# Kernel optimization log

Hardware: AMD Instinct MI355X
Metric: run time of the kernel (lower is better)

## Reference

```python
import jax, jax.numpy as jnp
import numpy as np

B, S, H = 64, 2048, 1024

def setup_inputs() -> dict:
    key = jax.random.key(0)
    k1, k2 = jax.random.split(key)
    enc_output = jax.random.normal(k1, (B, S, H), dtype=jnp.float32)
    h_n = jax.random.normal(k2, (B, H), dtype=jnp.float32)
    return {"enc_output": enc_output, "h_n": h_n}

def reference(enc_output, h_n):
    # dec_output: [B, 1, H]
    dec_output = h_n[:, None, :]
    # scores: [B, 1, S] = dec_output @ enc_output^T
    scores = jnp.einsum('bqh,bsh->bqs', dec_output, enc_output)
    attn = jax.nn.softmax(scores, axis=2)  # softmax over S
    # context: [B, 1, H] = attn @ enc_output
    context = jnp.einsum('bqs,bsh->bqh', attn, enc_output)
    # concat decoder state and attention context: [B, 1, 2H]
    return jnp.concatenate((dec_output, context), axis=2)
```

## Files before the change

kernel.cpp:

```cpp
#include <hip/hip_runtime.h>
#include <math.h>


#define BB 64
#define SS 2048
#define HH 1024
#define NCHUNK 16
#define SCHUNK (SS / NCHUNK)
#define NWAVE 4

typedef float fvec4 __attribute__((ext_vector_type(4)));

#define WS_ML_OFF ((size_t)BB * NCHUNK * HH)

__global__ __launch_bounds__(256) void attn_partial_kernel(
    const float* __restrict__ enc, const float* __restrict__ hn,
    float* __restrict__ ws)
{
    const int blk   = blockIdx.x;
    const int b     = blk / NCHUNK;
    const int chunk = blk % NCHUNK;
    const int tid   = threadIdx.x;
    const int wave  = tid >> 6;
    const int lane  = tid & 63;

    const fvec4* hn4 = (const fvec4*)(hn + (size_t)b * HH);
    fvec4 h4[4];
#pragma unroll
    for (int j = 0; j < 4; ++j) h4[j] = hn4[j * 64 + lane];

    const fvec4* enc4 = (const fvec4*)(enc + (size_t)b * SS * HH);

    float m = -INFINITY;
    float l = 0.0f;
    fvec4 acc[4];
#pragma unroll
    for (int j = 0; j < 4; ++j) acc[j] = (fvec4)(0.f, 0.f, 0.f, 0.f);

    const int s0    = chunk * SCHUNK;
    const int start = (blk * 53) & (SCHUNK - 1);

    for (int k = 0; k < SCHUNK / NWAVE; ++k) {
        const int r = (start + wave + NWAVE * k) & (SCHUNK - 1);
        const fvec4* row = enc4 + (size_t)(s0 + r) * (HH / 4);
        fvec4 e[4];
#pragma unroll
        for (int j = 0; j < 4; ++j)
            e[j] = __builtin_nontemporal_load(&row[j * 64 + lane]);

        float d = 0.0f;
#pragma unroll
        for (int j = 0; j < 4; ++j) {
            d += e[j].x * h4[j].x + e[j].y * h4[j].y
               + e[j].z * h4[j].z + e[j].w * h4[j].w;
        }
#pragma unroll
        for (int off = 32; off > 0; off >>= 1)
            d += __shfl_xor(d, off, 64);

        const float m_new = fmaxf(m, d);
        const float scale = __expf(m - m_new);
        const float p     = __expf(d - m_new);
        l = l * scale + p;
#pragma unroll
        for (int j = 0; j < 4; ++j) {
            acc[j].x = acc[j].x * scale + p * e[j].x;
            acc[j].y = acc[j].y * scale + p * e[j].y;
            acc[j].z = acc[j].z * scale + p * e[j].z;
            acc[j].w = acc[j].w * scale + p * e[j].w;
        }
        m = m_new;
    }

    __shared__ float s_m[NWAVE];
    __shared__ float s_l[NWAVE];
    __shared__ float s_acc[NWAVE][HH];

#pragma unroll
    for (int j = 0; j < 4; ++j)
        ((fvec4*)s_acc[wave])[j * 64 + lane] = acc[j];
    if (lane == 0) { s_m[wave] = m; s_l[wave] = l; }
    __syncthreads();

    float M = fmaxf(fmaxf(s_m[0], s_m[1]), fmaxf(s_m[2], s_m[3]));
    float sc[NWAVE];
    float L = 0.0f;
#pragma unroll
    for (int w = 0; w < NWAVE; ++w) {
        sc[w] = __expf(s_m[w] - M);
        L += s_l[w] * sc[w];
    }

    fvec4 ctx = (fvec4)(0.f, 0.f, 0.f, 0.f);
#pragma unroll
    for (int w = 0; w < NWAVE; ++w) {
        fvec4 a = ((const fvec4*)s_acc[w])[tid];
        ctx.x += sc[w] * a.x;  ctx.y += sc[w] * a.y;
        ctx.z += sc[w] * a.z;  ctx.w += sc[w] * a.w;
    }
    ((fvec4*)(ws + (size_t)blk * HH))[tid] = ctx;
    if (tid == 0) {
        ws[WS_ML_OFF + (size_t)blk * 2 + 0] = M;
        ws[WS_ML_OFF + (size_t)blk * 2 + 1] = L;
    }
}

__global__ __launch_bounds__(256) void attn_final_kernel(
    const float* __restrict__ hn, const float* __restrict__ ws,
    float* __restrict__ out)
{
    const int b   = blockIdx.x;
    const int tid = threadIdx.x;
    const float* ml = ws + WS_ML_OFF + (size_t)b * NCHUNK * 2;

    float M = -INFINITY;
#pragma unroll
    for (int c = 0; c < NCHUNK; ++c) M = fmaxf(M, ml[c * 2]);

    float sc[NCHUNK];
    float T = 0.0f;
#pragma unroll
    for (int c = 0; c < NCHUNK; ++c) {
        sc[c] = __expf(ml[c * 2] - M);
        T += sc[c] * ml[c * 2 + 1];
    }
    const float invT = 1.0f / T;

    fvec4 ctx = (fvec4)(0.f, 0.f, 0.f, 0.f);
#pragma unroll
    for (int c = 0; c < NCHUNK; ++c) {
        fvec4 a = ((const fvec4*)(ws + (size_t)(b * NCHUNK + c) * HH))[tid];
        ctx.x += sc[c] * a.x;  ctx.y += sc[c] * a.y;
        ctx.z += sc[c] * a.z;  ctx.w += sc[c] * a.w;
    }
    ctx.x *= invT; ctx.y *= invT; ctx.z *= invT; ctx.w *= invT;

    const fvec4 dec = ((const fvec4*)(hn + (size_t)b * HH))[tid];
    fvec4* o = (fvec4*)(out + (size_t)b * 2 * HH);
    o[tid]            = dec;
    o[tid + (HH / 4)] = ctx;
}

extern "C" void kernel_launch(void* const* d_in, const int* in_sizes, int n_in,
                              void* d_out, int out_size, void* d_ws, size_t ws_size,
                              hipStream_t stream) {
    const float* enc = (const float*)d_in[0];
    const float* hn  = (const float*)d_in[1];
    float* out = (float*)d_out;
    float* ws  = (float*)d_ws;

    attn_partial_kernel<<<dim3(BB * NCHUNK), dim3(256), 0, stream>>>(enc, hn, ws);
    attn_final_kernel<<<dim3(BB), dim3(256), 0, stream>>>(hn, ws, out);
}
```

Measured before the change: 642.2 us.

## Double-buffer row pairs and skip rescale when running max unchanged

Measured after the change: 644.4 us. About the same (+0.4%).

```diff
diff --git a/kernel.cpp b/kernel.cpp
--- a/kernel.cpp
+++ b/kernel.cpp
@@ -8,10 +8,63 @@
 #define NCHUNK 16
 #define SCHUNK (SS / NCHUNK)
 #define NWAVE 4
+#define NPAIR (SCHUNK / (2 * NWAVE))
 
 typedef float fvec4 __attribute__((ext_vector_type(4)));
 
 #define WS_ML_OFF ((size_t)BB * NCHUNK * HH)
+
+#define LOADP(kk, E0, E1) do {                                              \
+    const int pp_ = wave + NWAVE * (kk);                                    \
+    const int r0_ = (start + 2 * pp_)     & (SCHUNK - 1);                   \
+    const int r1_ = (start + 2 * pp_ + 1) & (SCHUNK - 1);                   \
+    const fvec4* R0_ = enc4 + (size_t)(s0 + r0_) * (HH / 4);                \
+    const fvec4* R1_ = enc4 + (size_t)(s0 + r1_) * (HH / 4);                \
+    _Pragma("unroll")                                                       \
+    for (int j = 0; j < 4; ++j) {                                           \
+        E0[j] = __builtin_nontemporal_load(&R0_[j * 64 + lane]);            \
+        E1[j] = __builtin_nontemporal_load(&R1_[j * 64 + lane]);            \
+    }                                                                       \
+} while (0)
+
+#define DOT4(E, j) (E[j].x * h4[j].x + E[j].y * h4[j].y                     \
+                  + E[j].z * h4[j].z + E[j].w * h4[j].w)
+
+#define CONSUME(E0, E1) do {                                                \
+    float d0_ = DOT4(E0, 0) + DOT4(E0, 1) + DOT4(E0, 2) + DOT4(E0, 3);     \
+    float d1_ = DOT4(E1, 0) + DOT4(E1, 1) + DOT4(E1, 2) + DOT4(E1, 3);     \
+    _Pragma("unroll")                                                       \
+    for (int off_ = 32; off_ > 0; off_ >>= 1) {                             \
+        d0_ += __shfl_xor(d0_, off_, 64);                                   \
+        d1_ += __shfl_xor(d1_, off_, 64);                                   \
+    }                                                                       \
+    const float pm_ = fmaxf(d0_, d1_);                                      \
+    if (pm_ <= m) {             \
+        const float p0_ = __expf(d0_ - m);                                  \
+        const float p1_ = __expf(d1_ - m);                                  \
+        l += p0_ + p1_;                                                     \
+        _Pragma("unroll")                                                   \
+        for (int j = 0; j < 4; ++j) {                                       \
+            acc[j].x = fmaf(p0_, E0[j].x, fmaf(p1_, E1[j].x, acc[j].x));    \
+            acc[j].y = fmaf(p0_, E0[j].y, fmaf(p1_, E1[j].y, acc[j].y));    \
+            acc[j].z = fmaf(p0_, E0[j].z, fmaf(p1_, E1[j].z, acc[j].z));    \
+            acc[j].w = fmaf(p0_, E0[j].w, fmaf(p1_, E1[j].w, acc[j].w));    \
+        }                                                                   \
+    } else {                    \
+        const float sc_ = __expf(m - pm_);     \
+        const float p0_ = __expf(d0_ - pm_);                                \
+        const float p1_ = __expf(d1_ - pm_);                                \
+        l = l * sc_ + p0_ + p1_;                                            \
+        m = pm_;                                                            \
+        _Pragma("unroll")                                                   \
+        for (int j = 0; j < 4; ++j) {                                       \
+            acc[j].x = fmaf(acc[j].x, sc_, fmaf(p0_, E0[j].x, p1_ * E1[j].x)); \
+            acc[j].y = fmaf(acc[j].y, sc_, fmaf(p0_, E0[j].y, p1_ * E1[j].y)); \
+            acc[j].z = fmaf(acc[j].z, sc_, fmaf(p0_, E0[j].z, p1_ * E1[j].z)); \
+            acc[j].w = fmaf(acc[j].w, sc_, fmaf(p0_, E0[j].w, p1_ * E1[j].w)); \
+        }                                                                   \
+    }                                                                       \
+} while (0)
 
 __global__ __launch_bounds__(256) void attn_partial_kernel(
     const float* __restrict__ enc, const float* __restrict__ hn,
@@ -40,37 +93,19 @@
     const int s0    = chunk * SCHUNK;
     const int start = (blk * 53) & (SCHUNK - 1);
 
-    for (int k = 0; k < SCHUNK / NWAVE; ++k) {
-        const int r = (start + wave + NWAVE * k) & (SCHUNK - 1);
-        const fvec4* row = enc4 + (size_t)(s0 + r) * (HH / 4);
-        fvec4 e[4];
+    fvec4 eA0[4], eA1[4], eB0[4], eB1[4];
+
+    LOADP(0, eA0, eA1);
 #pragma unroll
-        for (int j = 0; j < 4; ++j)
-            e[j] = __builtin_nontemporal_load(&row[j * 64 + lane]);
-
-        float d = 0.0f;
-#pragma unroll
-        for (int j = 0; j < 4; ++j) {
-            d += e[j].x * h4[j].x + e[j].y * h4[j].y
-               + e[j].z * h4[j].z + e[j].w * h4[j].w;
-        }
-#pragma unroll
-        for (int off = 32; off > 0; off >>= 1)
-            d += __shfl_xor(d, off, 64);
-
-        const float m_new = fmaxf(m, d);
-        const float scale = __expf(m - m_new);
-        const float p     = __expf(d - m_new);
-        l = l * scale + p;
-#pragma unroll
-        for (int j = 0; j < 4; ++j) {
-            acc[j].x = acc[j].x * scale + p * e[j].x;
-            acc[j].y = acc[j].y * scale + p * e[j].y;
-            acc[j].z = acc[j].z * scale + p * e[j].z;
-            acc[j].w = acc[j].w * scale + p * e[j].w;
-        }
-        m = m_new;
+    for (int k = 0; k < NPAIR / 2 - 1; ++k) {
+        LOADP(2 * k + 1, eB0, eB1);
+        CONSUME(eA0, eA1);
+        LOADP(2 * k + 2, eA0, eA1);
+        CONSUME(eB0, eB1);
     }
+    LOADP(NPAIR - 1, eB0, eB1);
+    CONSUME(eA0, eA1);
+    CONSUME(eB0, eB1);
 
     __shared__ float s_m[NWAVE];
     __shared__ float s_l[NWAVE];
```

## Double chunk count, give each wave a contiguous row run, branch online softmax

Applied to the files above, without the earlier changes.

Measured after the change: 659.2 us. +2.7%, slower.

```diff
diff --git a/kernel.cpp b/kernel.cpp
--- a/kernel.cpp
+++ b/kernel.cpp
@@ -5,9 +5,10 @@
 #define BB 64
 #define SS 2048
 #define HH 1024
-#define NCHUNK 16
+#define NCHUNK 32
 #define SCHUNK (SS / NCHUNK)
 #define NWAVE 4
+#define RUN (SCHUNK / NWAVE)
 
 typedef float fvec4 __attribute__((ext_vector_type(4)));
 
@@ -18,8 +19,8 @@
     float* __restrict__ ws)
 {
     const int blk   = blockIdx.x;
-    const int b     = blk / NCHUNK;
-    const int chunk = blk % NCHUNK;
+    const int b     = blk >> 5;
+    const int chunk = blk & (NCHUNK - 1);
     const int tid   = threadIdx.x;
     const int wave  = tid >> 6;
     const int lane  = tid & 63;
@@ -37,12 +38,12 @@
 #pragma unroll
     for (int j = 0; j < 4; ++j) acc[j] = (fvec4)(0.f, 0.f, 0.f, 0.f);
 
-    const int s0    = chunk * SCHUNK;
-    const int start = (blk * 53) & (SCHUNK - 1);
+    const int rowbase = chunk * SCHUNK + wave * RUN;
+    const int start   = (blk * 53 + wave * 29) & (RUN - 1);
 
-    for (int k = 0; k < SCHUNK / NWAVE; ++k) {
-        const int r = (start + wave + NWAVE * k) & (SCHUNK - 1);
-        const fvec4* row = enc4 + (size_t)(s0 + r) * (HH / 4);
+    for (int i = 0; i < RUN; ++i) {
+        const int r = rowbase + ((start + i) & (RUN - 1));
+        const fvec4* row = enc4 + (size_t)r * (HH / 4);
         fvec4 e[4];
 #pragma unroll
         for (int j = 0; j < 4; ++j)
@@ -58,18 +59,28 @@
         for (int off = 32; off > 0; off >>= 1)
             d += __shfl_xor(d, off, 64);
 
-        const float m_new = fmaxf(m, d);
-        const float scale = __expf(m - m_new);
-        const float p     = __expf(d - m_new);
-        l = l * scale + p;
+        if (d <= m) {
+            const float p = __expf(d - m);
+            l += p;
 #pragma unroll
-        for (int j = 0; j < 4; ++j) {
-            acc[j].x = acc[j].x * scale + p * e[j].x;
-            acc[j].y = acc[j].y * scale + p * e[j].y;
-            acc[j].z = acc[j].z * scale + p * e[j].z;
-            acc[j].w = acc[j].w * scale + p * e[j].w;
+            for (int j = 0; j < 4; ++j) {
+                acc[j].x = fmaf(p, e[j].x, acc[j].x);
+                acc[j].y = fmaf(p, e[j].y, acc[j].y);
+                acc[j].z = fmaf(p, e[j].z, acc[j].z);
+                acc[j].w = fmaf(p, e[j].w, acc[j].w);
+            }
+        } else {
+            const float sc = __expf(m - d);
+            l = fmaf(l, sc, 1.0f);
+            m = d;
+#pragma unroll
+            for (int j = 0; j < 4; ++j) {
+                acc[j].x = fmaf(acc[j].x, sc, e[j].x);
+                acc[j].y = fmaf(acc[j].y, sc, e[j].y);
+                acc[j].z = fmaf(acc[j].z, sc, e[j].z);
+                acc[j].w = fmaf(acc[j].w, sc, e[j].w);
+            }
         }
-        m = m_new;
     }
 
     __shared__ float s_m[NWAVE];
@@ -83,20 +94,20 @@
     __syncthreads();
 
     float M = fmaxf(fmaxf(s_m[0], s_m[1]), fmaxf(s_m[2], s_m[3]));
-    float sc[NWAVE];
+    float sc2[NWAVE];
     float L = 0.0f;
 #pragma unroll
     for (int w = 0; w < NWAVE; ++w) {
-        sc[w] = __expf(s_m[w] - M);
-        L += s_l[w] * sc[w];
+        sc2[w] = __expf(s_m[w] - M);
+        L += s_l[w] * sc2[w];
     }
 
     fvec4 ctx = (fvec4)(0.f, 0.f, 0.f, 0.f);
 #pragma unroll
     for (int w = 0; w < NWAVE; ++w) {
         fvec4 a = ((const fvec4*)s_acc[w])[tid];
-        ctx.x += sc[w] * a.x;  ctx.y += sc[w] * a.y;
-        ctx.z += sc[w] * a.z;  ctx.w += sc[w] * a.w;
+        ctx.x += sc2[w] * a.x;  ctx.y += sc2[w] * a.y;
+        ctx.z += sc2[w] * a.z;  ctx.w += sc2[w] * a.w;
     }
     ((fvec4*)(ws + (size_t)blk * HH))[tid] = ctx;
     if (tid == 0) {
```
